# Performance work log

Hardware: AMD Instinct MI355X
Metric: run time of the kernel (lower is better)

The kernel has to match this reference:

```python
import jax, jax.numpy as jnp
import numpy as np

N_NODES = 50000
N_EDGES = 800000
D_IN = 64
D_OUT = 64


def setup_inputs() -> dict:
    key = jax.random.key(0)
    k1, k2, k3, k4, k5 = jax.random.split(key, 5)
    feat = jax.random.normal(k1, (N_NODES, D_IN), dtype=jnp.float32)
    # torch Linear layout: W [out_feats, in_feats]
    W = jax.random.normal(k2, (D_OUT, D_IN), dtype=jnp.float32) * (1.0 / np.sqrt(D_IN))
    b = jax.random.normal(k3, (D_OUT,), dtype=jnp.float32) * 0.01
    eps = jnp.zeros((1,), dtype=jnp.float32)
    src = jax.random.randint(k4, (N_EDGES,), 0, N_NODES, dtype=jnp.int32)
    dst = jax.random.randint(k5, (N_EDGES,), 0, N_NODES, dtype=jnp.int32)
    return {"feat": feat, "W": W, "b": b, "eps": eps, "src": src, "dst": dst}


def reference(feat, W, b, eps, src, dst):
    # message = feat[src]; sum-aggregate per destination node
    neigh = jax.ops.segment_sum(feat[src], dst, num_segments=N_NODES)  # [N, D_in]
    rst = (1.0 + eps) * feat + neigh                                   # eps-scaled residual
    out = rst @ W.T + b                                                # Linear (torch layout)
    return out
```

## Files before the change

### kernel.cpp

```cpp
#include <hip/hip_runtime.h>

constexpr int N_NODES = 50000;
constexpr int N_EDGES = 800000;
constexpr int D = 64;

constexpr int NREG = 256;
constexpr int RSZ = 196;
constexpr int EPB = 3136;
constexpr int NBINB = 256;
constexpr int CELLCAP = 64;
constexpr int RECAP = 4608;

constexpr int WS_CNT2 = 0;
constexpr int WS_RBUF = NREG * NBINB;
constexpr size_t WS_HB_BYTE = (size_t)(WS_RBUF + (size_t)NREG * NBINB * CELLCAP) * 4;

__device__ __forceinline__ ushort to_bf16(float x) {
  unsigned u = __float_as_uint(x);
  u += 0x7FFF + ((u >> 16) & 1);
  return (ushort)(u >> 16);
}
__device__ __forceinline__ float bf_lo(unsigned u) {
  return __uint_as_float(u << 16);
}
__device__ __forceinline__ float bf_hi(unsigned u) {
  return __uint_as_float(u & 0xFFFF0000u);
}

__global__ __launch_bounds__(1024) void prep_kernel(
    const float4* __restrict__ feat4, const int* __restrict__ src,
    const int* __restrict__ dst, ushort* __restrict__ hb,
    int* __restrict__ cnt2, unsigned* __restrict__ rbuf) {
  __shared__ int cur[NREG];
  __shared__ unsigned scell[NREG * CELLCAP];
  int tid = threadIdx.x, blk = blockIdx.x;
  if (tid < NREG) cur[tid] = 0;

  int e0 = blk * EPB + tid * 4;
  bool valid = (tid * 4 < EPB) && (e0 + 4 <= N_EDGES);
  int4 d4 = {0, 0, 0, 0}, s4 = {0, 0, 0, 0};
  if (valid) {
    d4 = *reinterpret_cast<const int4*>(dst + e0);
    s4 = *reinterpret_cast<const int4*>(src + e0);
  }

  for (int t = blk * 1024 + tid; t < N_NODES * D / 4; t += NBINB * 1024) {
    float4 f = feat4[t];
    ushort4 h;
    h.x = to_bf16(f.x); h.y = to_bf16(f.y);
    h.z = to_bf16(f.z); h.w = to_bf16(f.w);
    *reinterpret_cast<ushort4*>(hb + t * 4) = h;
  }
  __syncthreads();

  if (valid) {
    const int dd[4] = {d4.x, d4.y, d4.z, d4.w};
    const int ss[4] = {s4.x, s4.y, s4.z, s4.w};
#pragma unroll
    for (int k = 0; k < 4; ++k) {
      int r = dd[k] / RSZ;
      unsigned pk = ((unsigned)(dd[k] - r * RSZ) << 16) | (unsigned)ss[k];
      int p = atomicAdd(&cur[r], 1);
      if (p < CELLCAP) scell[r * CELLCAP + p] = pk;
    }
  }
  __syncthreads();

  {
    int cell = tid >> 2, sub = tid & 3;
    int c = cur[cell];
    if (c > CELLCAP) c = CELLCAP;
    unsigned* gp = rbuf + (size_t)(cell * NBINB + blk) * CELLCAP;
    const unsigned* sp = scell + cell * CELLCAP;
    for (int i = sub * 4; i < c; i += 16)
      *reinterpret_cast<uint4*>(gp + i) = *reinterpret_cast<const uint4*>(sp + i);
  }
  if (tid < NREG) {
    int c = cur[tid];
    cnt2[tid * NBINB + blk] = (c > CELLCAP) ? CELLCAP : c;
  }
}

__global__ __launch_bounds__(1024) void gin_kernel(
    const float* __restrict__ feat, const ushort* __restrict__ hb,
    const float* __restrict__ W, const float* __restrict__ b,
    const float* __restrict__ eps, const int* __restrict__ cnt2,
    const unsigned* __restrict__ rbuf, float* __restrict__ out) {
  __shared__ float Wt[D * D];
  __shared__ unsigned ebuf[RECAP];
  __shared__ ushort sorted[RECAP];
  __shared__ int cellstart[NBINB + 1];
  __shared__ int hist[RSZ], nstart[RSZ + 1], cursor[RSZ];
  __shared__ int wsum[4], wsum2[4];
  __shared__ int wq;

  int tid = threadIdx.x, r = blockIdx.x;
  int lane = tid & 63, wv = tid >> 6;
  for (int q = tid; q < D * D; q += 1024) Wt[q] = W[((q & 63) << 6) + (q >> 6)];
  if (tid < RSZ) hist[tid] = 0;
  if (tid == 0) wq = 0;

  int c = (tid < NBINB) ? cnt2[r * NBINB + tid] : 0;
  int inc = c;
#pragma unroll
  for (int dlt = 1; dlt < 64; dlt <<= 1) {
    int t = __shfl_up(inc, (unsigned)dlt, 64);
    if (lane >= dlt) inc += t;
  }
  if (tid < 256 && lane == 63) wsum[wv] = inc;
  __syncthreads();
  if (tid < 256) {
    int prefix = inc - c;
    if (wv > 0) prefix += wsum[0];
    if (wv > 1) prefix += wsum[1];
    if (wv > 2) prefix += wsum[2];
    if (tid < NBINB) cellstart[tid] = prefix;
  }
  if (tid == 0) cellstart[NBINB] = wsum[0] + wsum[1] + wsum[2] + wsum[3];
  __syncthreads();
  int T = cellstart[NBINB];
  if (T > RECAP) T = RECAP;

  {
    int cell = tid >> 2, sub = tid & 3;
    if (cell < NBINB) {
      int cs = cellstart[cell];
      int cc = cellstart[cell + 1] - cs;
      const unsigned* cp = rbuf + (size_t)(r * NBINB + cell) * CELLCAP;
      for (int i = sub * 4; i < cc; i += 16) {
        uint4 v = *reinterpret_cast<const uint4*>(cp + i);
        if (cs + i + 0 < T && i + 0 < cc) ebuf[cs + i + 0] = v.x;
        if (cs + i + 1 < T && i + 1 < cc) ebuf[cs + i + 1] = v.y;
        if (cs + i + 2 < T && i + 2 < cc) ebuf[cs + i + 2] = v.z;
        if (cs + i + 3 < T && i + 3 < cc) ebuf[cs + i + 3] = v.w;
      }
    }
  }
  __syncthreads();

  for (int e = tid; e < T; e += 1024) atomicAdd(&hist[ebuf[e] >> 16], 1);
  __syncthreads();

  int h = (tid < RSZ) ? hist[tid] : 0;
  int inc2 = h;
#pragma unroll
  for (int dlt = 1; dlt < 64; dlt <<= 1) {
    int t = __shfl_up(inc2, (unsigned)dlt, 64);
    if (lane >= dlt) inc2 += t;
  }
  if (tid < 256 && lane == 63) wsum2[wv] = inc2;
  __syncthreads();
  if (tid < 256) {
    int prefix = inc2 - h;
    if (wv > 0) prefix += wsum2[0];
    if (wv > 1) prefix += wsum2[1];
    if (wv > 2) prefix += wsum2[2];
    if (tid < RSZ) {
      nstart[tid] = prefix;
      cursor[tid] = prefix;
    }
  }
  if (tid == 0) nstart[RSZ] = wsum2[0] + wsum2[1] + wsum2[2] + wsum2[3];
  __syncthreads();
  for (int e = tid; e < T; e += 1024) {
    unsigned pk = ebuf[e];
    int p = atomicAdd(&cursor[pk >> 16], 1);
    sorted[p] = (ushort)(pk & 0xFFFFu);
  }
  __syncthreads();

  int j8 = (tid & 7) << 3;
  float s = 1.0f + eps[0];

  for (;;) {
    int n = 0;
    if ((tid & 7) == 0) n = atomicAdd(&wq, 1);
    n = __shfl(n, 0, 8);
    if (n >= RSZ) break;

    int node = r * RSZ + n;
    if (node >= N_NODES) continue;

    float acc[8];
    {
      const float4 fa = *reinterpret_cast<const float4*>(feat + (node << 6) + j8);
      const float4 fb = *reinterpret_cast<const float4*>(feat + (node << 6) + j8 + 4);
      acc[0] = s * fa.x; acc[1] = s * fa.y; acc[2] = s * fa.z; acc[3] = s * fa.w;
      acc[4] = s * fb.x; acc[5] = s * fb.y; acc[6] = s * fb.z; acc[7] = s * fb.w;
    }

    int e = nstart[n], e1 = nstart[n + 1];
    for (; e + 8 <= e1; e += 8) {
      int i0 = sorted[e + 0], i1 = sorted[e + 1], i2 = sorted[e + 2], i3 = sorted[e + 3];
      int i4_ = sorted[e + 4], i5 = sorted[e + 5], i6 = sorted[e + 6], i7 = sorted[e + 7];
      const uint4 h0 = *reinterpret_cast<const uint4*>(hb + (i0 << 6) + j8);
      const uint4 h1 = *reinterpret_cast<const uint4*>(hb + (i1 << 6) + j8);
      const uint4 h2 = *reinterpret_cast<const uint4*>(hb + (i2 << 6) + j8);
      const uint4 h3 = *reinterpret_cast<const uint4*>(hb + (i3 << 6) + j8);
      const uint4 h4 = *reinterpret_cast<const uint4*>(hb + (i4_ << 6) + j8);
      const uint4 h5 = *reinterpret_cast<const uint4*>(hb + (i5 << 6) + j8);
      const uint4 h6 = *reinterpret_cast<const uint4*>(hb + (i6 << 6) + j8);
      const uint4 h7 = *reinterpret_cast<const uint4*>(hb + (i7 << 6) + j8);
      acc[0] += (bf_lo(h0.x) + bf_lo(h1.x)) + (bf_lo(h2.x) + bf_lo(h3.x))
              + (bf_lo(h4.x) + bf_lo(h5.x)) + (bf_lo(h6.x) + bf_lo(h7.x));
      acc[1] += (bf_hi(h0.x) + bf_hi(h1.x)) + (bf_hi(h2.x) + bf_hi(h3.x))
              + (bf_hi(h4.x) + bf_hi(h5.x)) + (bf_hi(h6.x) + bf_hi(h7.x));
      acc[2] += (bf_lo(h0.y) + bf_lo(h1.y)) + (bf_lo(h2.y) + bf_lo(h3.y))
              + (bf_lo(h4.y) + bf_lo(h5.y)) + (bf_lo(h6.y) + bf_lo(h7.y));
      acc[3] += (bf_hi(h0.y) + bf_hi(h1.y)) + (bf_hi(h2.y) + bf_hi(h3.y))
              + (bf_hi(h4.y) + bf_hi(h5.y)) + (bf_hi(h6.y) + bf_hi(h7.y));
      acc[4] += (bf_lo(h0.z) + bf_lo(h1.z)) + (bf_lo(h2.z) + bf_lo(h3.z))
              + (bf_lo(h4.z) + bf_lo(h5.z)) + (bf_lo(h6.z) + bf_lo(h7.z));
      acc[5] += (bf_hi(h0.z) + bf_hi(h1.z)) + (bf_hi(h2.z) + bf_hi(h3.z))
              + (bf_hi(h4.z) + bf_hi(h5.z)) + (bf_hi(h6.z) + bf_hi(h7.z));
      acc[6] += (bf_lo(h0.w) + bf_lo(h1.w)) + (bf_lo(h2.w) + bf_lo(h3.w))
              + (bf_lo(h4.w) + bf_lo(h5.w)) + (bf_lo(h6.w) + bf_lo(h7.w));
      acc[7] += (bf_hi(h0.w) + bf_hi(h1.w)) + (bf_hi(h2.w) + bf_hi(h3.w))
              + (bf_hi(h4.w) + bf_hi(h5.w)) + (bf_hi(h6.w) + bf_hi(h7.w));
    }
    for (; e < e1; ++e) {
      int sn = sorted[e];
      const uint4 hv = *reinterpret_cast<const uint4*>(hb + (sn << 6) + j8);
      acc[0] += bf_lo(hv.x); acc[1] += bf_hi(hv.x);
      acc[2] += bf_lo(hv.y); acc[3] += bf_hi(hv.y);
      acc[4] += bf_lo(hv.z); acc[5] += bf_hi(hv.z);
      acc[6] += bf_lo(hv.w); acc[7] += bf_hi(hv.w);
    }

    float res[8];
    {
      const float4 ba = *reinterpret_cast<const float4*>(b + j8);
      const float4 bb = *reinterpret_cast<const float4*>(b + j8 + 4);
      res[0] = ba.x; res[1] = ba.y; res[2] = ba.z; res[3] = ba.w;
      res[4] = bb.x; res[5] = bb.y; res[6] = bb.z; res[7] = bb.w;
    }
#pragma unroll
    for (int i = 0; i < D; ++i) {
      float rv = __shfl(acc[i & 7], i >> 3, 8);
      const float4 wa = *reinterpret_cast<const float4*>(Wt + i * D + j8);
      const float4 wb = *reinterpret_cast<const float4*>(Wt + i * D + j8 + 4);
      res[0] += rv * wa.x; res[1] += rv * wa.y;
      res[2] += rv * wa.z; res[3] += rv * wa.w;
      res[4] += rv * wb.x; res[5] += rv * wb.y;
      res[6] += rv * wb.z; res[7] += rv * wb.w;
    }
    float4 o0, o1;
    o0.x = res[0]; o0.y = res[1]; o0.z = res[2]; o0.w = res[3];
    o1.x = res[4]; o1.y = res[5]; o1.z = res[6]; o1.w = res[7];
    *reinterpret_cast<float4*>(out + (node << 6) + j8) = o0;
    *reinterpret_cast<float4*>(out + (node << 6) + j8 + 4) = o1;
  }
}

extern "C" void kernel_launch(void* const* d_in, const int* in_sizes, int n_in,
                              void* d_out, int out_size, void* d_ws, size_t ws_size,
                              hipStream_t stream) {
  const float* feat = (const float*)d_in[0];
  const float* W    = (const float*)d_in[1];
  const float* b    = (const float*)d_in[2];
  const float* eps  = (const float*)d_in[3];
  const int*   src  = (const int*)d_in[4];
  const int*   dst  = (const int*)d_in[5];
  float* out = (float*)d_out;

  int* ws = (int*)d_ws;
  int* cnt2      = ws + WS_CNT2;
  unsigned* rbuf = (unsigned*)(ws + WS_RBUF);
  ushort* hb     = (ushort*)((char*)d_ws + WS_HB_BYTE);

  hipLaunchKernelGGL(prep_kernel, dim3(NBINB), dim3(1024), 0, stream,
                     (const float4*)feat, src, dst, hb, cnt2, rbuf);
  hipLaunchKernelGGL(gin_kernel, dim3(NREG), dim3(1024), 0, stream,
                     feat, hb, W, b, eps, cnt2, rbuf, out);
}
```

Measured before the change: 106.4 us.

## Compute output Linear with bf16 MFMA using split-precision weights

Replaces the per-thread scalar FMA matvec, which used shuffles and reads of an fp32 transposed W in shared memory, with a block-wide 16x16x32 bf16 MFMA GEMM. Aggregated node rows are rounded to bf16 and staged in shared memory, reusing the edge buffer space. W is split into high and low bf16 parts so the weights keep extra precision. This lowers ALU and LDS traffic in the epilogue. In exchange it adds a block barrier, rounds the activations to bf16 (a precision loss), and writes output as scattered scalar stores.

New measurement: 102.3 us. -3.8%, faster.

```diff
diff --git a/kernel.cpp b/kernel.cpp
--- a/kernel.cpp
+++ b/kernel.cpp
@@ -11,9 +11,14 @@
 constexpr int CELLCAP = 64;
 constexpr int RECAP = 4608;
 
+constexpr int MT = 13;
+
 constexpr int WS_CNT2 = 0;
 constexpr int WS_RBUF = NREG * NBINB;
 constexpr size_t WS_HB_BYTE = (size_t)(WS_RBUF + (size_t)NREG * NBINB * CELLCAP) * 4;
+
+typedef __attribute__((ext_vector_type(8))) short short8v;
+typedef __attribute__((ext_vector_type(4))) float f32x4;
 
 __device__ __forceinline__ ushort to_bf16(float x) {
   unsigned u = __float_as_uint(x);
@@ -25,6 +30,9 @@
 }
 __device__ __forceinline__ float bf_hi(unsigned u) {
   return __uint_as_float(u & 0xFFFF0000u);
+}
+__device__ __forceinline__ float bf_val(ushort h) {
+  return __uint_as_float(((unsigned)h) << 16);
 }
 
 __global__ __launch_bounds__(1024) void prep_kernel(
@@ -86,9 +94,13 @@
     const float* __restrict__ W, const float* __restrict__ b,
     const float* __restrict__ eps, const int* __restrict__ cnt2,
     const unsigned* __restrict__ rbuf, float* __restrict__ out) {
-  __shared__ float Wt[D * D];
-  __shared__ unsigned ebuf[RECAP];
+  __shared__ __align__(16) char pool[MT * 16 * 72 * 2];
+  unsigned* ebuf = reinterpret_cast<unsigned*>(pool);
+  ushort* rstH = reinterpret_cast<ushort*>(pool);
   __shared__ ushort sorted[RECAP];
+  __shared__ ushort WbH[8 * 64 * 8];
+  __shared__ ushort WbL[8 * 64 * 8];
+  __shared__ float b_lds[D];
   __shared__ int cellstart[NBINB + 1];
   __shared__ int hist[RSZ], nstart[RSZ + 1], cursor[RSZ];
   __shared__ int wsum[4], wsum2[4];
@@ -96,7 +108,31 @@
 
   int tid = threadIdx.x, r = blockIdx.x;
   int lane = tid & 63, wv = tid >> 6;
-  for (int q = tid; q < D * D; q += 1024) Wt[q] = W[((q & 63) << 6) + (q >> 6)];
+
+  if (tid < 512) {
+    int tile = tid >> 6, l = tid & 63;
+    int tk = tile >> 2, tn = tile & 3;
+    int n = tn * 16 + (l & 15);
+    int kb = tk * 32 + ((l >> 4) << 3);
+    const float4 w0 = *reinterpret_cast<const float4*>(W + (n << 6) + kb);
+    const float4 w1 = *reinterpret_cast<const float4*>(W + (n << 6) + kb + 4);
+    float wf[8] = {w0.x, w0.y, w0.z, w0.w, w1.x, w1.y, w1.z, w1.w};
+    ushort hh[8], ll[8];
+#pragma unroll
+    for (int e = 0; e < 8; ++e) {
+      ushort h = to_bf16(wf[e]);
+      hh[e] = h;
+      ll[e] = to_bf16(wf[e] - bf_val(h));
+    }
+    uint4 vH, vL;
+    vH.x = hh[0] | ((unsigned)hh[1] << 16); vH.y = hh[2] | ((unsigned)hh[3] << 16);
+    vH.z = hh[4] | ((unsigned)hh[5] << 16); vH.w = hh[6] | ((unsigned)hh[7] << 16);
+    vL.x = ll[0] | ((unsigned)ll[1] << 16); vL.y = ll[2] | ((unsigned)ll[3] << 16);
+    vL.z = ll[4] | ((unsigned)ll[5] << 16); vL.w = ll[6] | ((unsigned)ll[7] << 16);
+    *reinterpret_cast<uint4*>(&WbH[(tile * 64 + l) * 8]) = vH;
+    *reinterpret_cast<uint4*>(&WbL[(tile * 64 + l) * 8]) = vL;
+  }
+  if (tid < D) b_lds[tid] = b[tid];
   if (tid < RSZ) hist[tid] = 0;
   if (tid == 0) wq = 0;
 
@@ -227,28 +263,39 @@
       acc[6] += bf_lo(hv.w); acc[7] += bf_hi(hv.w);
     }
 
-    float res[8];
-    {
-      const float4 ba = *reinterpret_cast<const float4*>(b + j8);
-      const float4 bb = *reinterpret_cast<const float4*>(b + j8 + 4);
-      res[0] = ba.x; res[1] = ba.y; res[2] = ba.z; res[3] = ba.w;
-      res[4] = bb.x; res[5] = bb.y; res[6] = bb.z; res[7] = bb.w;
-    }
-#pragma unroll
-    for (int i = 0; i < D; ++i) {
-      float rv = __shfl(acc[i & 7], i >> 3, 8);
-      const float4 wa = *reinterpret_cast<const float4*>(Wt + i * D + j8);
-      const float4 wb = *reinterpret_cast<const float4*>(Wt + i * D + j8 + 4);
-      res[0] += rv * wa.x; res[1] += rv * wa.y;
-      res[2] += rv * wa.z; res[3] += rv * wa.w;
-      res[4] += rv * wb.x; res[5] += rv * wb.y;
-      res[6] += rv * wb.z; res[7] += rv * wb.w;
-    }
-    float4 o0, o1;
-    o0.x = res[0]; o0.y = res[1]; o0.z = res[2]; o0.w = res[3];
-    o1.x = res[4]; o1.y = res[5]; o1.z = res[6]; o1.w = res[7];
-    *reinterpret_cast<float4*>(out + (node << 6) + j8) = o0;
-    *reinterpret_cast<float4*>(out + (node << 6) + j8 + 4) = o1;
+    unsigned p0 = (unsigned)to_bf16(acc[0]) | ((unsigned)to_bf16(acc[1]) << 16);
+    unsigned p1 = (unsigned)to_bf16(acc[2]) | ((unsigned)to_bf16(acc[3]) << 16);
+    unsigned p2 = (unsigned)to_bf16(acc[4]) | ((unsigned)to_bf16(acc[5]) << 16);
+    unsigned p3 = (unsigned)to_bf16(acc[6]) | ((unsigned)to_bf16(acc[7]) << 16);
+    uint4 vv; vv.x = p0; vv.y = p1; vv.z = p2; vv.w = p3;
+    *reinterpret_cast<uint4*>(&rstH[n * 72 + j8]) = vv;
+  }
+  __syncthreads();
+
+  {
+    int l = tid & 63;
+    int lr = l & 15, lc = l >> 4;
+    for (int t = wv; t < MT * 4; t += 16) {
+      int mt = t >> 2, nt = t & 3;
+      int m0 = mt << 4, n0 = nt << 4;
+      float bc = b_lds[n0 + lr];
+      f32x4 cacc = {bc, bc, bc, bc};
+#pragma unroll
+      for (int tk = 0; tk < 2; ++tk) {
+        short8v a = *reinterpret_cast<const short8v*>(&rstH[(m0 + lr) * 72 + tk * 32 + lc * 8]);
+        short8v wh = *reinterpret_cast<const short8v*>(&WbH[((tk * 4 + nt) * 64 + l) * 8]);
+        short8v wl = *reinterpret_cast<const short8v*>(&WbL[((tk * 4 + nt) * 64 + l) * 8]);
+        cacc = __builtin_amdgcn_mfma_f32_16x16x32_bf16(a, wh, cacc, 0, 0, 0);
+        cacc = __builtin_amdgcn_mfma_f32_16x16x32_bf16(a, wl, cacc, 0, 0, 0);
+      }
+#pragma unroll
+      for (int rr = 0; rr < 4; ++rr) {
+        int row = m0 + lc * 4 + rr;
+        int node = r * RSZ + row;
+        if (row < RSZ && node < N_NODES)
+          out[(node << 6) + n0 + lr] = cacc[rr];
+      }
+    }
   }
 }
 
```
